# Kernel tuning notes

Hardware: AMD Instinct MI355X
Metric: run time of the kernel (lower is better)

Reference implementation:

```python
import jax, jax.numpy as jnp
import numpy as np
import math

NTOKEN, NINP, NHID, SEQ, BATCH = 33278, 400, 1150, 70, 16
ODE_STEPS = 8  # fixed-step RK4 over t in [0,1] (reference for the adaptive solver)


def lstm_layer(x, h0, c0, Wih, Whh, bih, bhh):
    # x: [S, B, in]; PyTorch gate order i, f, g, o
    def step(carry, xt):
        h, c = carry
        g = xt @ Wih.T + h @ Whh.T + bih + bhh
        i, f, gg, o = jnp.split(g, 4, axis=-1)
        c = jax.nn.sigmoid(f) * c + jax.nn.sigmoid(i) * jnp.tanh(gg)
        h = jax.nn.sigmoid(o) * jnp.tanh(c)
        return (h, c), h
    (hT, cT), ys = jax.lax.scan(step, (h0, c0), x)
    return ys, hT, cT


def cnf_delta_logp(E, cnf_W, cnf_b):
    # ODEnet: f(t,z) = relu(Linear(concat([t, z]))); exact divergence since
    # Jacobian diag = relu'(pre) * diag(Wx). Integrates dz/dt=f, d(dlogp)/dt=-div f.
    wt = cnf_W[:, 0]
    Wx = cnf_W[:, 1:]
    dWx = jnp.diag(Wx)

    def f(t, z):
        pre = z @ Wx.T + t * wt + cnf_b          # [ntoken, ninp]
        div = jnp.sum((pre > 0) * dWx, axis=-1)  # exact trace of df/dz
        return jax.nn.relu(pre), -div

    dt = 1.0 / ODE_STEPS

    def rk4(carry, t):
        z, dl = carry
        k1z, k1l = f(t, z)
        k2z, k2l = f(t + dt / 2, z + dt / 2 * k1z)
        k3z, k3l = f(t + dt / 2, z + dt / 2 * k2z)
        k4z, k4l = f(t + dt, z + dt * k3z)
        z = z + dt / 6 * (k1z + 2 * k2z + 2 * k3z + k4z)
        dl = dl + dt / 6 * (k1l + 2 * k2l + 2 * k3l + k4l)
        return (z, dl), None

    ts = jnp.arange(ODE_STEPS, dtype=E.dtype) * dt
    (zT, dl), _ = jax.lax.scan(rk4, (E, jnp.zeros(E.shape[0], E.dtype)), ts)
    return dl  # [ntoken]


def setup_inputs() -> dict:
    key = jax.random.key(0)
    ks = jax.random.split(key, 16)
    s = 0.1
    inp = {
        "tokens": jax.random.randint(ks[0], (SEQ, BATCH), 0, NTOKEN),
        "h0_0": jnp.zeros((BATCH, NHID), jnp.float32),
        "c0_0": jnp.zeros((BATCH, NHID), jnp.float32),
        "h0_1": jnp.zeros((BATCH, NHID), jnp.float32),
        "c0_1": jnp.zeros((BATCH, NHID), jnp.float32),
        "h0_2": jnp.zeros((BATCH, NINP), jnp.float32),
        "c0_2": jnp.zeros((BATCH, NINP), jnp.float32),
        "emb_W": jax.random.uniform(ks[1], (NTOKEN, NINP), jnp.float32, -s, s),
        "Wih0": jax.random.normal(ks[2], (4 * NHID, NINP), jnp.float32) * 0.02,
        "Whh0": jax.random.normal(ks[3], (4 * NHID, NHID), jnp.float32) * 0.02,
        "bih0": jnp.zeros((4 * NHID,), jnp.float32),
        "bhh0": jnp.zeros((4 * NHID,), jnp.float32),
        "Wih1": jax.random.normal(ks[4], (4 * NHID, NHID), jnp.float32) * 0.02,
        "Whh1": jax.random.normal(ks[5], (4 * NHID, NHID), jnp.float32) * 0.02,
        "bih1": jnp.zeros((4 * NHID,), jnp.float32),
        "bhh1": jnp.zeros((4 * NHID,), jnp.float32),
        "Wih2": jax.random.normal(ks[6], (4 * NINP, NHID), jnp.float32) * 0.02,
        "Whh2": jax.random.normal(ks[7], (4 * NINP, NINP), jnp.float32) * 0.02,
        "bih2": jnp.zeros((4 * NINP,), jnp.float32),
        "bhh2": jnp.zeros((4 * NINP,), jnp.float32),
        "cnf_W": jax.random.normal(ks[8], (NINP, NINP + 1), jnp.float32) * 0.05,
        "cnf_b": jnp.zeros((NINP,), jnp.float32),
    }
    return inp


def reference(tokens, h0_0, c0_0, h0_1, c0_1, h0_2, c0_2, emb_W,
              Wih0, Whh0, bih0, bhh0, Wih1, Whh1, bih1, bhh1,
              Wih2, Whh2, bih2, bhh2, cnf_W, cnf_b):
    # embedding (eval mode: all dropouts are identity)
    x = emb_W[tokens]                               # [S, B, ninp]
    x, h1, c1 = lstm_layer(x, h0_0, c0_0, Wih0, Whh0, bih0, bhh0)
    x, h2, c2 = lstm_layer(x, h0_1, c0_1, Wih1, Whh1, bih1, bhh1)
    x, h3, c3 = lstm_layer(x, h0_2, c0_2, Wih2, Whh2, bih2, bhh2)
    # nhidlast == ninp -> no latent projection
    h = x.reshape(SEQ * BATCH, NINP)

    # MVNLogProb vectorized: -0.5 ||E_v - h_i||^2 - k/2 log(2*pi)
    e2 = jnp.sum(emb_W * emb_W, axis=-1)            # [ntoken]
    h2n = jnp.sum(h * h, axis=-1, keepdims=True)    # [SB, 1]
    sq = e2[None, :] - 2.0 * (h @ emb_W.T) + h2n    # [SB, ntoken]
    log_pz0 = -0.5 * sq - (NINP / 2.0) * math.log(2.0 * math.pi)

    # CNF delta_logp is identical for every token position (loop-invariant)
    delta = cnf_delta_logp(emb_W, cnf_W, cnf_b)     # [ntoken]
    log_pz1 = log_pz0 - delta[None, :]

    prob = jax.nn.softmax(log_pz1, axis=-1)
    log_prob = jnp.log(prob + 1e-8)
    model_output = log_prob.reshape(SEQ, BATCH, NTOKEN)
    return model_output, h1, c1, h2, c2, h3, c3
```

## Files before the change

### kernel.cpp

```cpp
#include <hip/hip_runtime.h>
#include <hip/hip_bf16.h>
#include <math.h>

#define SEQL 70
#define NTOK 33278
#define ODE_STEPS 8
#define NBLK 242
#define NGRP 16
#define CZS 418

typedef __attribute__((ext_vector_type(4))) float f32x4;
typedef __attribute__((ext_vector_type(8))) short s16x8;
typedef unsigned short u16;

__device__ __forceinline__ u16 f2b(float f) {
    union { float f; unsigned int u; } a; a.f = f;
    unsigned int u = a.u;
    return (u16)((u + 0x7FFFu + ((u >> 16) & 1u)) >> 16);
}
__device__ __forceinline__ float b2f(u16 s) {
    union { unsigned int u; float f; } a; a.u = ((unsigned int)s) << 16;
    return a.f;
}

__device__ __forceinline__ unsigned czoff(int row, int colb) {
    unsigned s = ((colb < 768 ? (row & 7) : (row & 3)) << 4);
    return (unsigned)(row * 832 + (colb ^ (int)s));
}

__global__ void cvt_pad_k(const float* __restrict__ src, u16* __restrict__ dst,
                          int G, int Nin, int Nop, int Kin, int Kp, int rs, int co) {
    size_t total = (size_t)G * Nop * Kp;
    for (size_t idx = (size_t)blockIdx.x * 256 + threadIdx.x; idx < total;
         idx += (size_t)gridDim.x * 256) {
        int k = (int)(idx % Kp);
        size_t t2 = idx / Kp;
        int j = (int)(t2 % Nop);
        int g = (int)(t2 / Nop);
        float v = 0.f;
        if (j < Nin && k < Kin) v = src[((size_t)g * Nin + j) * rs + co + k];
        dst[idx] = f2b(v);
// ... 55 lines not shown
                          float* __restrict__ C, int Kp, int lda, int ldb, int ldc,
                          int Mreal, int Nreal, const float* __restrict__ uvec) {
    const int tid = threadIdx.x;
    const int wid = tid >> 6, lane = tid & 63;
    const int la = lane & 15, lk = (lane >> 4) * 8;
    const int m0 = blockIdx.y * 64 + wid * 16;
    const int n0 = blockIdx.x * 64;
    const f32x4 Z4 = {0.f, 0.f, 0.f, 0.f};
    f32x4 acc[4] = {Z4, Z4, Z4, Z4};
    const u16* Ar = A + (size_t)(m0 + la) * lda + lk;
    const u16* Br = B + (size_t)(n0 + la) * ldb + lk;
    for (int k = 0; k < Kp; k += 32) {
        s16x8 a = *(const s16x8*)(Ar + k);
#pragma unroll
        for (int nt = 0; nt < 4; ++nt) {
            s16x8 b = *(const s16x8*)(Br + (size_t)nt * 16 * ldb + k);
            acc[nt] = __builtin_amdgcn_mfma_f32_16x16x32_bf16(a, b, acc[nt], 0, 0, 0);
        }
    }
    const int mr = m0 + (lane >> 4) * 4;
#pragma unroll
    for (int nt = 0; nt < 4; ++nt) {
        int cc = n0 + nt * 16 + la;
        if (cc >= Nreal) continue;
        float uv = uvec ? uvec[cc] : 0.f;
#pragma unroll
        for (int r = 0; r < 4; ++r) {
            int rr = mr + r;
            if (rr < Mreal) C[(size_t)rr * ldc + cc] = acc[nt][r] + uv;
        }
    }
}

__device__ __forceinline__ void gridbar(int* base, int nb, int iter) {
    __syncthreads();
    if (threadIdx.x == 0) {
        int grp = blockIdx.x & (NGRP - 1);
        int gsz = nb / NGRP + ((grp < (nb % NGRP)) ? 1 : 0);
        int* gc   = base + grp * 16;
        int* root = base + 256;
        int* gen  = base + 272;
        int old = __hip_atomic_fetch_add(gc, 1, __ATOMIC_ACQ_REL, __HIP_MEMORY_SCOPE_AGENT);
        if ((old % gsz) == gsz - 1) {
            int r = __hip_atomic_fetch_add(root, 1, __ATOMIC_ACQ_REL, __HIP_MEMORY_SCOPE_AGENT);
            if ((r % NGRP) == NGRP - 1)
                __hip_atomic_fetch_add(gen, 1, __ATOMIC_ACQ_REL, __HIP_MEMORY_SCOPE_AGENT);
        }
        while (__hip_atomic_load(gen, __ATOMIC_RELAXED, __HIP_MEMORY_SCOPE_AGENT) <= iter)
            __builtin_amdgcn_s_sleep(8);
        (void)__hip_atomic_load(gen, __ATOMIC_ACQUIRE, __HIP_MEMORY_SCOPE_AGENT);
    }
    __syncthreads();
}

__global__ __launch_bounds__(768, 3) void lstm_k(
    const float* __restrict__ c00, const float* __restrict__ c01,
    const float* __restrict__ c02,
    const u16* __restrict__ Whh0p, const u16* __restrict__ Wih1p,
    const u16* __restrict__ Whh1p, const u16* __restrict__ Wih2p,
    const u16* __restrict__ Whh2p,
    const float* __restrict__ xW0, const float* __restrict__ bias2v,
    const float* __restrict__ bias1v,
    u16* __restrict__ ys0s, u16* __restrict__ ys1s, u16* __restrict__ ys2s,
    float* __restrict__ oh1, float* __restrict__ oc1,
    float* __restrict__ oh2, float* __restrict__ oc2,
    float* __restrict__ oh3, float* __restrict__ oc3,
    int* __restrict__ bar)
{
    __shared__ __align__(16) char smem[162816];
    u16* wlds = (u16*)smem;
    float* gl = (float*)(smem + 147456);
    const int tid = threadIdx.x;
    const int bid = blockIdx.x;
    const int wv = tid >> 6, lane = tid & 63;
    const int la = lane & 15, lg = lane >> 4;

    int role, jb;
    if (bid < 72) { role = 0; jb = bid; }
    else if (bid < 216) { role = 1; jb = bid - 72; }
    else { role = 2; jb = bid - 216; }

    if (role == 0) {
        for (int s = tid; s < 4 * 36 * 64; s += 768) {
            int ln = s & 63, kt = (s >> 6) % 36, nt = s / (36 * 64);
            int row = nt * 1152 + jb * 16 + (ln & 15);
            int col = kt * 32 + (ln >> 4) * 8;
            *(s16x8*)(wlds + (size_t)s * 8) =
                *(const s16x8*)(Whh0p + (size_t)row * 1152 + col);
        }
    } else if (role == 1) {
        for (int s = tid; s < 2 * 72 * 64; s += 768) {
            int ln = s & 63, kt = (s >> 6) % 72, nt = s / (72 * 64);
            int lr = nt * 16 + (ln & 15);
            int row = (lr >> 3) * 1152 + jb * 8 + (lr & 7);
            int col8 = (ln >> 4) * 8;
            const u16* src = (kt < 36)
                ? Wih1p + (size_t)row * 1152 + kt * 32 + col8
                : Whh1p + (size_t)row * 1152 + (kt - 36) * 32 + col8;
            *(s16x8*)(wlds + (size_t)s * 8) = *(const s16x8*)src;
        }
    }
    __syncthreads();

    float c_reg = 0.f;
    for (int sg = 0; sg < 72; ++sg) {
        int t = sg - role;
        if (t >= 0 && t < SEQL) {
            f32x4 acc = {0.f, 0.f, 0.f, 0.f};
            if (role == 0) {
                int nt = wv / 3, kg = wv - nt * 3;
                const u16* ar = ys0s + ((size_t)sg * 16 + la) * 1152 + lg * 8;
                for (int kt = kg * 12; kt < kg * 12 + 12; ++kt) {
                    s16x8 a = *(const s16x8*)(ar + kt * 32);
                    s16x8 b = *(const s16x8*)(wlds + ((size_t)(nt * 36 + kt) * 64 + lane) * 8);
                    acc = __builtin_amdgcn_mfma_f32_16x16x32_bf16(a, b, acc, 0, 0, 0);
                }
                *(f32x4*)(gl + wv * 320 + la * 20 + lg * 4) = acc;
            } else if (role == 1) {
                int nt = wv / 6, kg = wv - nt * 6;
                const u16* ax = ys0s + ((size_t)sg * 16 + la) * 1152 + lg * 8;
                const u16* ah = ys1s + ((size_t)(sg - 1) * 16 + la) * 1152 + lg * 8;
                for (int kt = kg * 12; kt < kg * 12 + 12; ++kt) {
                    s16x8 a = (kt < 36) ? *(const s16x8*)(ax + kt * 32)
                                        : *(const s16x8*)(ah + (kt - 36) * 32);
                    s16x8 b = *(const s16x8*)(wlds + ((size_t)(nt * 72 + kt) * 64 + lane) * 8);
                    acc = __builtin_amdgcn_mfma_f32_16x16x32_bf16(a, b, acc, 0, 0, 0);
                }
                *(f32x4*)(gl + wv * 320 + la * 20 + lg * 4) = acc;
            } else {
                int nt = wv / 3, kg = wv - nt * 3;
                int k0 = (kg * 49) / 3, k1 = ((kg + 1) * 49) / 3;
                const u16* ax = ys1s + ((size_t)(sg - 1) * 16 + la) * 1152 + lg * 8;
                const u16* ah = ys2s + ((size_t)(sg - 2) * 16 + la) * 416 + lg * 8;
                int wr = nt * 416 + jb * 16 + la;
                for (int kt = k0; kt < k1; ++kt) {
                    s16x8 a, b;
                    if (kt < 36) {
                        a = *(const s16x8*)(ax + kt * 32);
                        b = *(const s16x8*)(Wih2p + (size_t)wr * 1152 + kt * 32 + lg * 8);
                    } else {
                        a = *(const s16x8*)(ah + (kt - 36) * 32);
                        b = *(const s16x8*)(Whh2p + (size_t)wr * 416 + (kt - 36) * 32 + lg * 8);
                    }
                    acc = __builtin_amdgcn_mfma_f32_16x16x32_bf16(a, b, acc, 0, 0, 0);
                }
                *(f32x4*)(gl + wv * 320 + la * 20 + lg * 4) = acc;
            }
            __syncthreads();
            if (role == 1) {
                if (tid < 128) {
                    int u = tid & 7, tb = tid >> 3;
                    int ug = jb * 8 + u;
                    float gv[4];
#pragma unroll
                    for (int g = 0; g < 4; ++g) {
                        int lr = g * 8 + u;
                        int nt = lr >> 4, li = lr & 15;
                        float s = 0.f;
#pragma unroll
                        for (int kg = 0; kg < 6; ++kg)
                            s += gl[(nt * 6 + kg) * 320 + li * 20 + tb];
                        gv[g] = s + bias1v[g * 1152 + ug];
                    }
                    float cprev = (t == 0) ? ((ug < 1150) ? c01[tb * 1150 + ug] : 0.f) : c_reg;
                    float si = 1.f / (1.f + expf(-gv[0]));
                    float sf = 1.f / (1.f + expf(-gv[1]));
                    float so = 1.f / (1.f + expf(-gv[3]));
                    float cn = sf * cprev + si * tanhf(gv[2]);
                    float hn = so * tanhf(cn);
                    c_reg = cn;
                    if (ug < 1150) {
                        ys1s[((size_t)sg * 16 + tb) * 1152 + ug] = f2b(hn);
                        if (t == SEQL - 1) { oh2[tb * 1150 + ug] = hn; oc2[tb * 1150 + ug] = cn; }
                    }
                }
            } else if (tid < 256) {
                int u = tid & 15, tb = tid >> 4;
                int ug = jb * 16 + u;
                float gv[4];
#pragma unroll
                for (int g = 0; g < 4; ++g) {
                    float s = 0.f;
#pragma unroll
                    for (int kg = 0; kg < 3; ++kg)
                        s += gl[(g * 3 + kg) * 320 + u * 20 + tb];
                    gv[g] = s + ((role == 0)
                                 ? xW0[((size_t)t * 16 + tb) * 4608 + g * 1152 + ug]
                                 : bias2v[g * 416 + ug]);
                }
                int N = (role == 0) ? 1150 : 400;
                const float* c0i = (role == 0) ? c00 : c02;
                float cprev = (t == 0) ? ((ug < N) ? c0i[tb * N + ug] : 0.f) : c_reg;
                float si = 1.f / (1.f + expf(-gv[0]));
                float sf = 1.f / (1.f + expf(-gv[1]));
                float so = 1.f / (1.f + expf(-gv[3]));
                float cn = sf * cprev + si * tanhf(gv[2]);
                float hn = so * tanhf(cn);
                c_reg = cn;
                if (ug < N) {
                    if (role == 0) {
                        ys0s[((size_t)(sg + 1) * 16 + tb) * 1152 + ug] = f2b(hn);
                        if (t == SEQL - 1) { oh1[tb * 1150 + ug] = hn; oc1[tb * 1150 + ug] = cn; }
                    } else {
                        ys2s[((size_t)(sg - 1) * 16 + tb) * 416 + ug] = f2b(hn);
                        if (t == SEQL - 1) { oh3[tb * 400 + ug] = hn; oc3[tb * 400 + ug] = cn; }
                    }
                }
            }
        }
        gridbar(bar, NBLK, sg);
    }
}

__global__ __launch_bounds__(512, 2) void cnf_k(const float* __restrict__ emb,
                                                const u16* __restrict__ Wxp,
                                                const float* __restrict__ wt,
                                                const float* __restrict__ bv,
                                                const float* __restrict__ dwx,
                                                float* __restrict__ dl) {
    __shared__ float z0s[64 * CZS];
    __shared__ __align__(16) u16 zi[64 * 416];
    const int tid = threadIdx.x;
    const int m0 = blockIdx.x * 64;

    for (int idx = tid; idx < 64 * 416; idx += 512) {
        int r = idx / 416, cc = idx - r * 416;
        int row = m0 + r;
        float v = (cc < 400 && row < NTOK) ? emb[(size_t)row * 400 + cc] : 0.f;
        if (cc < 416) z0s[r * CZS + cc] = v;
        *(u16*)((char*)zi + czoff(r, cc * 2)) = f2b(v);
    }

    const int wv = tid >> 6, lane = tid & 63;
    const int la = lane & 15, lg = lane >> 4;
    const int lk = lg * 8;
    const int Qw = (wv == 0) ? 4 : 3;
    const int ntb = (wv == 0) ? 0 : 4 + (wv - 1) * 3;

    float wtq[4], bq[4], dwq[4];
#pragma unroll
    for (int q = 0; q < 4; ++q) {
        if (q < Qw) {
            int col = (ntb + q) * 16 + la;
            wtq[q] = wt[col]; bq[q] = bv[col]; dwq[q] = dwx[col];
        } else { wtq[q] = 0.f; bq[q] = 0.f; dwq[q] = 0.f; }
    }
    __syncthreads();

    const float dt = 1.f / ODE_STEPS;
    const f32x4 Z4 = {0.f, 0.f, 0.f, 0.f};
    float Aacc[4][4][4];
#pragma unroll
    for (int m = 0; m < 4; ++m)
#pragma unroll
        for (int q = 0; q < 4; ++q)
#pragma unroll
            for (int r = 0; r < 4; ++r) Aacc[m][q][r] = 0.f;
    float divp[4][4];
#pragma unroll
    for (int m = 0; m < 4; ++m)
#pragma unroll
        for (int r = 0; r < 4; ++r) divp[m][r] = 0.f;

#pragma unroll 1
    for (int st = 0; st < ODE_STEPS; ++st) {
        float t0 = st * dt;
#pragma unroll 1
        for (int s = 0; s < 4; ++s) {
            float ts = t0 + ((s == 0) ? 0.f : (s == 3) ? dt : 0.5f * dt);
            float wgt = (s == 1 || s == 2) ? 2.f : 1.f;
            float cs = (s == 2) ? dt : 0.5f * dt;
            f32x4 pre[4][4];
#pragma unroll
            for (int m = 0; m < 4; ++m)
#pragma unroll
                for (int q = 0; q < 4; ++q) pre[m][q] = Z4;
#pragma unroll 1
            for (int kk = 0; kk < 13; ++kk) {
                s16x8 b[4];
#pragma unroll
                for (int q = 0; q < 4; ++q)
                    if (q < Qw)
                        b[q] = *(const s16x8*)(Wxp + (size_t)((ntb + q) * 16 + la) * 416 +
                                               kk * 32 + lk);
#pragma unroll
                for (int m = 0; m < 4; ++m) {
                    int row = m * 16 + la;
                    s16x8 a = *(const s16x8*)((const char*)zi + czoff(row, (kk * 64 + lg * 16)));
#pragma unroll
                    for (int q = 0; q < 4; ++q)
                        if (q < Qw)
                            pre[m][q] = __builtin_amdgcn_mfma_f32_16x16x32_bf16(
                                a, b[q], pre[m][q], 0, 0, 0);
                }
            }
            __syncthreads();
#pragma unroll
            for (int m = 0; m < 4; ++m) {
#pragma unroll
                for (int q = 0; q < 4; ++q) {
                    if (q >= Qw) continue;
                    int col = (ntb + q) * 16 + la;
#pragma unroll
                    for (int r = 0; r < 4; ++r) {
                        int row = m * 16 + lg * 4 + r;
                        float pv = pre[m][q][r] + ts * wtq[q] + bq[q];
                        float kz = fmaxf(pv, 0.f);
                        if (pv > 0.f) divp[m][r] += dwq[q] * wgt;
                        float An = Aacc[m][q][r] + wgt * kz;
                        float ev;
                        if (s < 3) {
                            Aacc[m][q][r] = An;
                            ev = z0s[row * CZS + col] + cs * kz;
                        } else {
                            float zn = z0s[row * CZS + col] + (dt / 6.f) * An;
                            z0s[row * CZS + col] = zn;
                            Aacc[m][q][r] = 0.f;
                            ev = zn;
                        }
                        *(u16*)((char*)zi + czoff(row, col * 2)) = f2b(ev);
                    }
                }
            }
            __syncthreads();
        }
    }

#pragma unroll
    for (int m = 0; m < 4; ++m)
#pragma unroll
        for (int r = 0; r < 4; ++r) {
            float v = divp[m][r];
            v += __shfl_xor(v, 1, 64);
            v += __shfl_xor(v, 2, 64);
            v += __shfl_xor(v, 4, 64);
            v += __shfl_xor(v, 8, 64);
            divp[m][r] = v;
        }
    float* dsc = (float*)zi;
    if (la == 0) {
#pragma unroll
        for (int m = 0; m < 4; ++m)
#pragma unroll
            for (int r = 0; r < 4; ++r)
                dsc[wv * 64 + m * 16 + lg * 4 + r] = divp[m][r];
    }
    __syncthreads();
    for (int row = tid; row < 64; row += 512) {
        float s = 0.f;
#pragma unroll
        for (int w = 0; w < 8; ++w) s += dsc[w * 64 + row];
        if (m0 + row < NTOK) dl[m0 + row] = -(dt / 6.f) * s;
    }
}

__global__ void logsoftmax_k(float* __restrict__ L, int n) {
    const int row = blockIdx.x;
    float* R = L + (size_t)row * n;
    const int tid = threadIdx.x;
    float mx = -INFINITY, s = 0.f;
    for (int c = tid; c < n; c += 256) {
        float v = R[c];
        float nm = fmaxf(mx, v);
        s = s * expf(mx - nm) + expf(v - nm);
        mx = nm;
    }
#pragma unroll
    for (int off = 1; off < 64; off <<= 1) {
        float om = __shfl_xor(mx, off, 64);
        float os = __shfl_xor(s, off, 64);
        float nm = fmaxf(mx, om);
        s = s * expf(mx - nm) + os * expf(om - nm);
        mx = nm;
    }
    __shared__ float smx[4], ssm[4];
    if ((tid & 63) == 0) { smx[tid >> 6] = mx; ssm[tid >> 6] = s; }
    __syncthreads();
    float bm = fmaxf(fmaxf(smx[0], smx[1]), fmaxf(smx[2], smx[3]));
    float bs = ssm[0] * expf(smx[0] - bm) + ssm[1] * expf(smx[1] - bm) +
               ssm[2] * expf(smx[2] - bm) + ssm[3] * expf(smx[3] - bm);
    float lz = logf(bs);
    for (int c = tid; c < n; c += 256) {
        float v = R[c];
        R[c] = logf(expf(v - bm) + 1e-8f * bs) - lz;
// ... 57 lines not shown
    int*   bar   = (int*)alloc(4096);

    size_t OM = (size_t)SEQL * 16 * NTOK;
    float* oh1 = out + OM;
    float* oc1 = oh1 + 16 * 1150;
    float* oh2 = oc1 + 16 * 1150;
    float* oc2 = oh2 + 16 * 1150;
    float* oh3 = oc2 + 16 * 1150;
    float* oc3 = oh3 + 16 * 400;

    hipMemsetAsync(bar, 0, 4096, stream);
    hipMemsetAsync(ys0s, 0, (size_t)1136 * 1152 * 2, stream);
    hipMemsetAsync(ys1s, 0, (size_t)1136 * 1152 * 2, stream);
    hipMemsetAsync(ys2s, 0, (size_t)1184 * 416 * 2, stream);

    cvt_pad_k<<<2048, 256, 0, stream>>>(Wih0, Wih0p, 4, 1150, 1152, 400, 416, 400, 0);
    cvt_pad_k<<<2048, 256, 0, stream>>>(Whh0, Whh0p, 4, 1150, 1152, 1150, 1152, 1150, 0);
    cvt_pad_k<<<2048, 256, 0, stream>>>(Wih1, Wih1p, 4, 1150, 1152, 1150, 1152, 1150, 0);
    cvt_pad_k<<<2048, 256, 0, stream>>>(Whh1, Whh1p, 4, 1150, 1152, 1150, 1152, 1150, 0);
    cvt_pad_k<<<2048, 256, 0, stream>>>(Wih2, Wih2p, 4, 400, 416, 1150, 1152, 1150, 0);
    cvt_pad_k<<<2048, 256, 0, stream>>>(Whh2, Whh2p, 4, 400, 416, 400, 416, 400, 0);
    cvt_pad_k<<<2048, 256, 0, stream>>>(embW, emb_p, 1, 33278, 33280, 400, 416, 400, 0);
    cvt_pad_k<<<2048, 256, 0, stream>>>(cnfW, Wxp, 1, 400, 416, 400, 416, 401, 1);
    bias_k<<<(4 * 1152 + 255) / 256, 256, 0, stream>>>(bih0, bhh0, bias0, 1150, 1152);
    bias_k<<<(4 * 1152 + 255) / 256, 256, 0, stream>>>(bih1, bhh1, bias1, 1150, 1152);
    bias_k<<<(4 * 416 + 255) / 256, 256, 0, stream>>>(bih2, bhh2, bias2, 400, 416);
    wtdwx_k<<<2, 256, 0, stream>>>(cnfW, wtv, dwx);
    rowsumsq_k<<<NTOK, 64, 0, stream>>>(embW, e2, 400);

    h0cvt_k<<<(16 * 1152 + 255) / 256, 256, 0, stream>>>(h00, ys0s, 1150, 1152);
    h0cvt_k<<<(16 * 1152 + 255) / 256, 256, 0, stream>>>(h01, ys1s, 1150, 1152);
    h0cvt_k<<<(16 * 416 + 255) / 256, 256, 0, stream>>>(h02, ys2s, 400, 416);

    cnf_k<<<520, 512, 0, stream>>>(embW, Wxp, wtv, cnfb, dwx, dl);
    ucomb_k<<<(NTOK + 255) / 256, 256, 0, stream>>>(e2, dl, uvec);

    embed_k<<<(1152 * 416 + 255) / 256, 256, 0, stream>>>(tokens, embW, x0);
    gemm_bt_k<<<dim3(72, 18), 256, 0, stream>>>(x0, Wih0p, xW, 416, 416, 416, 4608,
                                                1120, 4608, bias0);

    lstm_k<<<NBLK, 768, 0, stream>>>(
        c00, c01, c02, Whh0p, Wih1p, Whh1p, Wih2p, Whh2p,
        xW, bias2, bias1, ys0s, ys1s, ys2s,
        oh1, oc1, oh2, oc2, oh3, oc3, bar);

    gemm_bt_k<<<dim3(520, 18), 256, 0, stream>>>(ys2s + (size_t)16 * 416, emb_p, out,
                                                 416, 416, 416, NTOK, 1120, NTOK, uvec);
    logsoftmax_k<<<1120, 256, 0, stream>>>(out, NTOK);
}
```

Baseline: 2.998 ms.

## Replace global grid barrier with per-role barriers and generation-based dataflow waits

The LSTM persistent kernel drops the single grid-wide barrier per wavefront step. Each layer role now gets its own hierarchical barrier, and downstream layers spin on the upstream role's generation counter. Layers can therefore run ahead of one another instead of marching in lockstep. Separately, the CNF kernel uses 32-row tiles with twice as many blocks and a higher occupancy bound, to improve parallelism. The risks are ordering bugs: there is no back-pressure from downstream layers and the barrier-counter layout is new.

New measurement: 3.188 ms. 6.3% more time.

```diff
diff --git a/kernel.cpp b/kernel.cpp
--- a/kernel.cpp
+++ b/kernel.cpp
@@ -6,7 +6,6 @@
 #define NTOK 33278
 #define ODE_STEPS 8
 #define NBLK 242
-#define NGRP 16
 #define CZS 418
 
 typedef __attribute__((ext_vector_type(4))) float f32x4;
@@ -128,22 +127,30 @@
     }
 }
 
-__device__ __forceinline__ void gridbar(int* base, int nb, int iter) {
+__device__ __forceinline__ void rolebar(int* base, int nb, int ngrp, int roleBlk, int iter) {
     __syncthreads();
     if (threadIdx.x == 0) {
-        int grp = blockIdx.x & (NGRP - 1);
-        int gsz = nb / NGRP + ((grp < (nb % NGRP)) ? 1 : 0);
+        int grp = roleBlk % ngrp;
+        int gsz = nb / ngrp + ((grp < (nb % ngrp)) ? 1 : 0);
         int* gc   = base + grp * 16;
-        int* root = base + 256;
-        int* gen  = base + 272;
+        int* root = base + ngrp * 16;
+        int* gen  = base + ngrp * 16 + 16;
         int old = __hip_atomic_fetch_add(gc, 1, __ATOMIC_ACQ_REL, __HIP_MEMORY_SCOPE_AGENT);
         if ((old % gsz) == gsz - 1) {
             int r = __hip_atomic_fetch_add(root, 1, __ATOMIC_ACQ_REL, __HIP_MEMORY_SCOPE_AGENT);
-            if ((r % NGRP) == NGRP - 1)
+            if ((r % ngrp) == ngrp - 1)
                 __hip_atomic_fetch_add(gen, 1, __ATOMIC_ACQ_REL, __HIP_MEMORY_SCOPE_AGENT);
         }
         while (__hip_atomic_load(gen, __ATOMIC_RELAXED, __HIP_MEMORY_SCOPE_AGENT) <= iter)
-            __builtin_amdgcn_s_sleep(8);
+            __builtin_amdgcn_s_sleep(4);
+        (void)__hip_atomic_load(gen, __ATOMIC_ACQUIRE, __HIP_MEMORY_SCOPE_AGENT);
+    }
+    __syncthreads();
+}
+__device__ __forceinline__ void waitgen(int* gen, int needed) {
+    if (threadIdx.x == 0) {
+        while (__hip_atomic_load(gen, __ATOMIC_RELAXED, __HIP_MEMORY_SCOPE_AGENT) < needed)
+            __builtin_amdgcn_s_sleep(4);
         (void)__hip_atomic_load(gen, __ATOMIC_ACQUIRE, __HIP_MEMORY_SCOPE_AGENT);
     }
     __syncthreads();
@@ -176,6 +183,12 @@
     else if (bid < 216) { role = 1; jb = bid - 72; }
     else { role = 2; jb = bid - 216; }
 
+    int* bar0 = bar;
+    int* bar1 = bar + 256;
+    int* bar2 = bar + 768;
+    int* g0 = bar0 + 144;
+    int* g1 = bar1 + 272;
+
     if (role == 0) {
         for (int s = tid; s < 4 * 36 * 64; s += 768) {
             int ln = s & 63, kt = (s >> 6) % 36, nt = s / (36 * 64);
@@ -199,127 +212,129 @@
     __syncthreads();
 
     float c_reg = 0.f;
-    for (int sg = 0; sg < 72; ++sg) {
-        int t = sg - role;
-        if (t >= 0 && t < SEQL) {
-            f32x4 acc = {0.f, 0.f, 0.f, 0.f};
-            if (role == 0) {
-                int nt = wv / 3, kg = wv - nt * 3;
-                const u16* ar = ys0s + ((size_t)sg * 16 + la) * 1152 + lg * 8;
-                for (int kt = kg * 12; kt < kg * 12 + 12; ++kt) {
-                    s16x8 a = *(const s16x8*)(ar + kt * 32);
-                    s16x8 b = *(const s16x8*)(wlds + ((size_t)(nt * 36 + kt) * 64 + lane) * 8);
-                    acc = __builtin_amdgcn_mfma_f32_16x16x32_bf16(a, b, acc, 0, 0, 0);
+    for (int t = 0; t < SEQL; ++t) {
+        if (role == 1) waitgen(g0, t + 1);
+        else if (role == 2) waitgen(g1, t + 1);
+
+        f32x4 acc = {0.f, 0.f, 0.f, 0.f};
+        if (role == 0) {
+            int nt = wv / 3, kg = wv - nt * 3;
+            const u16* ar = ys0s + ((size_t)t * 16 + la) * 1152 + lg * 8;
+            for (int kt = kg * 12; kt < kg * 12 + 12; ++kt) {
+                s16x8 a = *(const s16x8*)(ar + kt * 32);
+                s16x8 b = *(const s16x8*)(wlds + ((size_t)(nt * 36 + kt) * 64 + lane) * 8);
+                acc = __builtin_amdgcn_mfma_f32_16x16x32_bf16(a, b, acc, 0, 0, 0);
+            }
+            *(f32x4*)(gl + wv * 320 + la * 20 + lg * 4) = acc;
+        } else if (role == 1) {
+            int nt = wv / 6, kg = wv - nt * 6;
+            const u16* ax = ys0s + ((size_t)(t + 1) * 16 + la) * 1152 + lg * 8;
+            const u16* ah = ys1s + ((size_t)t * 16 + la) * 1152 + lg * 8;
+            for (int kt = kg * 12; kt < kg * 12 + 12; ++kt) {
+                s16x8 a = (kt < 36) ? *(const s16x8*)(ax + kt * 32)
+                                    : *(const s16x8*)(ah + (kt - 36) * 32);
+                s16x8 b = *(const s16x8*)(wlds + ((size_t)(nt * 72 + kt) * 64 + lane) * 8);
+                acc = __builtin_amdgcn_mfma_f32_16x16x32_bf16(a, b, acc, 0, 0, 0);
+            }
+            *(f32x4*)(gl + wv * 320 + la * 20 + lg * 4) = acc;
+        } else {
+            int nt = wv / 3, kg = wv - nt * 3;
+            int k0 = (kg * 49) / 3, k1 = ((kg + 1) * 49) / 3;
+            const u16* ax = ys1s + ((size_t)(t + 1) * 16 + la) * 1152 + lg * 8;
+            const u16* ah = ys2s + ((size_t)t * 16 + la) * 416 + lg * 8;
+            int wr = nt * 416 + jb * 16 + la;
+            for (int kt = k0; kt < k1; ++kt) {
+                s16x8 a, b;
+                if (kt < 36) {
+                    a = *(const s16x8*)(ax + kt * 32);
+                    b = *(const s16x8*)(Wih2p + (size_t)wr * 1152 + kt * 32 + lg * 8);
+                } else {
+                    a = *(const s16x8*)(ah + (kt - 36) * 32);
+                    b = *(const s16x8*)(Whh2p + (size_t)wr * 416 + (kt - 36) * 32 + lg * 8);
                 }
-                *(f32x4*)(gl + wv * 320 + la * 20 + lg * 4) = acc;
-            } else if (role == 1) {
-                int nt = wv / 6, kg = wv - nt * 6;
-                const u16* ax = ys0s + ((size_t)sg * 16 + la) * 1152 + lg * 8;
-                const u16* ah = ys1s + ((size_t)(sg - 1) * 16 + la) * 1152 + lg * 8;
-                for (int kt = kg * 12; kt < kg * 12 + 12; ++kt) {
-                    s16x8 a = (kt < 36) ? *(const s16x8*)(ax + kt * 32)
-                                        : *(const s16x8*)(ah + (kt - 36) * 32);
-                    s16x8 b = *(const s16x8*)(wlds + ((size_t)(nt * 72 + kt) * 64 + lane) * 8);
-                    acc = __builtin_amdgcn_mfma_f32_16x16x32_bf16(a, b, acc, 0, 0, 0);
+                acc = __builtin_amdgcn_mfma_f32_16x16x32_bf16(a, b, acc, 0, 0, 0);
+            }
+            *(f32x4*)(gl + wv * 320 + la * 20 + lg * 4) = acc;
+        }
+        __syncthreads();
+        if (role == 1) {
+            if (tid < 128) {
+                int u = tid & 7, tb = tid >> 3;
+                int ug = jb * 8 + u;
+                float gv[4];
+#pragma unroll
+                for (int g = 0; g < 4; ++g) {
+                    int lr = g * 8 + u;
+                    int nt = lr >> 4, li = lr & 15;
+                    float s = 0.f;
+#pragma unroll
+                    for (int kg = 0; kg < 6; ++kg)
+                        s += gl[(nt * 6 + kg) * 320 + li * 20 + tb];
+                    gv[g] = s + bias1v[g * 1152 + ug];
                 }
-                *(f32x4*)(gl + wv * 320 + la * 20 + lg * 4) = acc;
-            } else {
-                int nt = wv / 3, kg = wv - nt * 3;
-                int k0 = (kg * 49) / 3, k1 = ((kg + 1) * 49) / 3;
-                const u16* ax = ys1s + ((size_t)(sg - 1) * 16 + la) * 1152 + lg * 8;
-                const u16* ah = ys2s + ((size_t)(sg - 2) * 16 + la) * 416 + lg * 8;
-                int wr = nt * 416 + jb * 16 + la;
-                for (int kt = k0; kt < k1; ++kt) {
-                    s16x8 a, b;
-                    if (kt < 36) {
-                        a = *(const s16x8*)(ax + kt * 32);
-                        b = *(const s16x8*)(Wih2p + (size_t)wr * 1152 + kt * 32 + lg * 8);
-                    } else {
-                        a = *(const s16x8*)(ah + (kt - 36) * 32);
-                        b = *(const s16x8*)(Whh2p + (size_t)wr * 416 + (kt - 36) * 32 + lg * 8);
-                    }
-                    acc = __builtin_amdgcn_mfma_f32_16x16x32_bf16(a, b, acc, 0, 0, 0);
-                }
-                *(f32x4*)(gl + wv * 320 + la * 20 + lg * 4) = acc;
-            }
-            __syncthreads();
-            if (role == 1) {
-                if (tid < 128) {
-                    int u = tid & 7, tb = tid >> 3;
-                    int ug = jb * 8 + u;
-                    float gv[4];
-#pragma unroll
-                    for (int g = 0; g < 4; ++g) {
-                        int lr = g * 8 + u;
-                        int nt = lr >> 4, li = lr & 15;
-                        float s = 0.f;
-#pragma unroll
-                        for (int kg = 0; kg < 6; ++kg)
-                            s += gl[(nt * 6 + kg) * 320 + li * 20 + tb];
-                        gv[g] = s + bias1v[g * 1152 + ug];
-                    }
-                    float cprev = (t == 0) ? ((ug < 1150) ? c01[tb * 1150 + ug] : 0.f) : c_reg;
-                    float si = 1.f / (1.f + expf(-gv[0]));
-                    float sf = 1.f / (1.f + expf(-gv[1]));
-                    float so = 1.f / (1.f + expf(-gv[3]));
-                    float cn = sf * cprev + si * tanhf(gv[2]);
-                    float hn = so * tanhf(cn);
-                    c_reg = cn;
-                    if (ug < 1150) {
-                        ys1s[((size_t)sg * 16 + tb) * 1152 + ug] = f2b(hn);
-                        if (t == SEQL - 1) { oh2[tb * 1150 + ug] = hn; oc2[tb * 1150 + ug] = cn; }
-                    }
-                }
-            } else if (tid < 256) {
-                int u = tid & 15, tb = tid >> 4;
-                int ug = jb * 16 + u;
-                float gv[4];
-#pragma unroll
-                for (int g = 0; g < 4; ++g) {
-                    float s = 0.f;
-#pragma unroll
-                    for (int kg = 0; kg < 3; ++kg)
-                        s += gl[(g * 3 + kg) * 320 + u * 20 + tb];
-                    gv[g] = s + ((role == 0)
-                                 ? xW0[((size_t)t * 16 + tb) * 4608 + g * 1152 + ug]
-                                 : bias2v[g * 416 + ug]);
-                }
-                int N = (role == 0) ? 1150 : 400;
-                const float* c0i = (role == 0) ? c00 : c02;
-                float cprev = (t == 0) ? ((ug < N) ? c0i[tb * N + ug] : 0.f) : c_reg;
+                float cprev = (t == 0) ? ((ug < 1150) ? c01[tb * 1150 + ug] : 0.f) : c_reg;
                 float si = 1.f / (1.f + expf(-gv[0]));
                 float sf = 1.f / (1.f + expf(-gv[1]));
                 float so = 1.f / (1.f + expf(-gv[3]));
                 float cn = sf * cprev + si * tanhf(gv[2]);
                 float hn = so * tanhf(cn);
                 c_reg = cn;
-                if (ug < N) {
-                    if (role == 0) {
-                        ys0s[((size_t)(sg + 1) * 16 + tb) * 1152 + ug] = f2b(hn);
-                        if (t == SEQL - 1) { oh1[tb * 1150 + ug] = hn; oc1[tb * 1150 + ug] = cn; }
-                    } else {
-                        ys2s[((size_t)(sg - 1) * 16 + tb) * 416 + ug] = f2b(hn);
-                        if (t == SEQL - 1) { oh3[tb * 400 + ug] = hn; oc3[tb * 400 + ug] = cn; }
-                    }
+                if (ug < 1150) {
+                    ys1s[((size_t)(t + 1) * 16 + tb) * 1152 + ug] = f2b(hn);
+                    if (t == SEQL - 1) { oh2[tb * 1150 + ug] = hn; oc2[tb * 1150 + ug] = cn; }
                 }
             }
-        }
-        gridbar(bar, NBLK, sg);
-    }
-}
-
-__global__ __launch_bounds__(512, 2) void cnf_k(const float* __restrict__ emb,
+        } else if (tid < 256) {
+            int u = tid & 15, tb = tid >> 4;
+            int ug = jb * 16 + u;
+            float gv[4];
+#pragma unroll
+            for (int g = 0; g < 4; ++g) {
+                float s = 0.f;
+#pragma unroll
+                for (int kg = 0; kg < 3; ++kg)
+                    s += gl[(g * 3 + kg) * 320 + u * 20 + tb];
+                gv[g] = s + ((role == 0)
+                             ? xW0[((size_t)t * 16 + tb) * 4608 + g * 1152 + ug]
+                             : bias2v[g * 416 + ug]);
+            }
+            int N = (role == 0) ? 1150 : 400;
+            const float* c0i = (role == 0) ? c00 : c02;
+            float cprev = (t == 0) ? ((ug < N) ? c0i[tb * N + ug] : 0.f) : c_reg;
+            float si = 1.f / (1.f + expf(-gv[0]));
+            float sf = 1.f / (1.f + expf(-gv[1]));
+            float so = 1.f / (1.f + expf(-gv[3]));
+            float cn = sf * cprev + si * tanhf(gv[2]);
+            float hn = so * tanhf(cn);
+            c_reg = cn;
+            if (ug < N) {
+                if (role == 0) {
+                    ys0s[((size_t)(t + 1) * 16 + tb) * 1152 + ug] = f2b(hn);
+                    if (t == SEQL - 1) { oh1[tb * 1150 + ug] = hn; oc1[tb * 1150 + ug] = cn; }
+                } else {
+                    ys2s[((size_t)(t + 1) * 16 + tb) * 416 + ug] = f2b(hn);
+                    if (t == SEQL - 1) { oh3[tb * 400 + ug] = hn; oc3[tb * 400 + ug] = cn; }
+                }
+            }
+        }
+        if (role == 0) rolebar(bar0, 72, 8, jb, t);
+        else if (role == 1) rolebar(bar1, 144, 16, jb, t);
+        else rolebar(bar2, 26, 1, jb, t);
+    }
+}
+
+__global__ __launch_bounds__(512, 4) void cnf_k(const float* __restrict__ emb,
                                                 const u16* __restrict__ Wxp,
                                                 const float* __restrict__ wt,
                                                 const float* __restrict__ bv,
                                                 const float* __restrict__ dwx,
                                                 float* __restrict__ dl) {
-    __shared__ float z0s[64 * CZS];
-    __shared__ __align__(16) u16 zi[64 * 416];
+    __shared__ float z0s[32 * CZS];
+    __shared__ __align__(16) u16 zi[32 * 416];
     const int tid = threadIdx.x;
-    const int m0 = blockIdx.x * 64;
-
-    for (int idx = tid; idx < 64 * 416; idx += 512) {
+    const int m0 = blockIdx.x * 32;
+
+    for (int idx = tid; idx < 32 * 416; idx += 512) {
         int r = idx / 416, cc = idx - r * 416;
         int row = m0 + r;
         float v = (cc < 400 && row < NTOK) ? emb[(size_t)row * 400 + cc] : 0.f;
@@ -345,16 +360,16 @@
 
     const float dt = 1.f / ODE_STEPS;
     const f32x4 Z4 = {0.f, 0.f, 0.f, 0.f};
-    float Aacc[4][4][4];
-#pragma unroll
-    for (int m = 0; m < 4; ++m)
+    float Aacc[2][4][4];
+#pragma unroll
+    for (int m = 0; m < 2; ++m)
 #pragma unroll
         for (int q = 0; q < 4; ++q)
 #pragma unroll
             for (int r = 0; r < 4; ++r) Aacc[m][q][r] = 0.f;
-    float divp[4][4];
-#pragma unroll
-    for (int m = 0; m < 4; ++m)
+    float divp[2][4];
+#pragma unroll
+    for (int m = 0; m < 2; ++m)
 #pragma unroll
         for (int r = 0; r < 4; ++r) divp[m][r] = 0.f;
 
@@ -366,9 +381,9 @@
             float ts = t0 + ((s == 0) ? 0.f : (s == 3) ? dt : 0.5f * dt);
             float wgt = (s == 1 || s == 2) ? 2.f : 1.f;
             float cs = (s == 2) ? dt : 0.5f * dt;
-            f32x4 pre[4][4];
-#pragma unroll
-            for (int m = 0; m < 4; ++m)
+            f32x4 pre[2][4];
+#pragma unroll
+            for (int m = 0; m < 2; ++m)
 #pragma unroll
                 for (int q = 0; q < 4; ++q) pre[m][q] = Z4;
 #pragma unroll 1
@@ -380,9 +395,9 @@
                         b[q] = *(const s16x8*)(Wxp + (size_t)((ntb + q) * 16 + la) * 416 +
                                                kk * 32 + lk);
 #pragma unroll
-                for (int m = 0; m < 4; ++m) {
+                for (int m = 0; m < 2; ++m) {
                     int row = m * 16 + la;
-                    s16x8 a = *(const s16x8*)((const char*)zi + czoff(row, (kk * 64 + lg * 16)));
+                    s16x8 a = *(const s16x8*)((const char*)zi + czoff(row, kk * 64 + lg * 16));
 #pragma unroll
                     for (int q = 0; q < 4; ++q)
                         if (q < Qw)
@@ -392,7 +407,7 @@
             }
             __syncthreads();
 #pragma unroll
-            for (int m = 0; m < 4; ++m) {
+            for (int m = 0; m < 2; ++m) {
 #pragma unroll
                 for (int q = 0; q < 4; ++q) {
                     if (q >= Qw) continue;
@@ -423,7 +438,7 @@
     }
 
 #pragma unroll
-    for (int m = 0; m < 4; ++m)
+    for (int m = 0; m < 2; ++m)
 #pragma unroll
         for (int r = 0; r < 4; ++r) {
             float v = divp[m][r];
@@ -436,16 +451,16 @@
     float* dsc = (float*)zi;
     if (la == 0) {
 #pragma unroll
-        for (int m = 0; m < 4; ++m)
+        for (int m = 0; m < 2; ++m)
 #pragma unroll
             for (int r = 0; r < 4; ++r)
-                dsc[wv * 64 + m * 16 + lg * 4 + r] = divp[m][r];
+                dsc[wv * 32 + m * 16 + lg * 4 + r] = divp[m][r];
     }
     __syncthreads();
-    for (int row = tid; row < 64; row += 512) {
+    for (int row = tid; row < 32; row += 512) {
         float s = 0.f;
 #pragma unroll
-        for (int w = 0; w < 8; ++w) s += dsc[w * 64 + row];
+        for (int w = 0; w < 8; ++w) s += dsc[w * 32 + row];
         if (m0 + row < NTOK) dl[m0 + row] = -(dt / 6.f) * s;
     }
 }
@@ -569,7 +584,7 @@
     h0cvt_k<<<(16 * 1152 + 255) / 256, 256, 0, stream>>>(h01, ys1s, 1150, 1152);
     h0cvt_k<<<(16 * 416 + 255) / 256, 256, 0, stream>>>(h02, ys2s, 400, 416);
 
-    cnf_k<<<520, 512, 0, stream>>>(embW, Wxp, wtv, cnfb, dwx, dl);
+    cnf_k<<<1040, 512, 0, stream>>>(embW, Wxp, wtv, cnfb, dwx, dl);
     ucomb_k<<<(NTOK + 255) / 256, 256, 0, stream>>>(e2, dl, uvec);
 
     embed_k<<<(1152 * 416 + 255) / 256, 256, 0, stream>>>(tokens, embW, x0);
```

## Replace global grid barrier with per-layer barriers and flag waits; widen CNF blocks

Applied to the files above, without the earlier changes.

The LSTM wavefront kernel drops its single hierarchical grid barrier across all 242 blocks. Each layer role now has its own flat barrier, and downstream layers spin on the upstream layer's generation counter, so layers can run ahead in a pipelined way instead of stepping in lockstep. The sleep interval is also shortened. Separately, the CNF kernel moves from 512 to 1024 threads per block, with fewer column tiles per wave. The barrier change relies on correct memory ordering across per-role counters, and the barrier buffer must be laid out and zeroed for the new counter offsets.

Measured after the change: 2.993 ms. No clear change (-0.2%).

```diff
diff --git a/kernel.cpp b/kernel.cpp
--- a/kernel.cpp
+++ b/kernel.cpp
@@ -6,7 +6,6 @@
 #define NTOK 33278
 #define ODE_STEPS 8
 #define NBLK 242
-#define NGRP 16
 #define CZS 418
 
 typedef __attribute__((ext_vector_type(4))) float f32x4;
@@ -128,22 +127,22 @@
     }
 }
 
-__device__ __forceinline__ void gridbar(int* base, int nb, int iter) {
+__device__ __forceinline__ void flatbar(int* cnt, int* gen, int nb, int iter) {
     __syncthreads();
     if (threadIdx.x == 0) {
-        int grp = blockIdx.x & (NGRP - 1);
-        int gsz = nb / NGRP + ((grp < (nb % NGRP)) ? 1 : 0);
-        int* gc   = base + grp * 16;
-        int* root = base + 256;
-        int* gen  = base + 272;
-        int old = __hip_atomic_fetch_add(gc, 1, __ATOMIC_ACQ_REL, __HIP_MEMORY_SCOPE_AGENT);
-        if ((old % gsz) == gsz - 1) {
-            int r = __hip_atomic_fetch_add(root, 1, __ATOMIC_ACQ_REL, __HIP_MEMORY_SCOPE_AGENT);
-            if ((r % NGRP) == NGRP - 1)
-                __hip_atomic_fetch_add(gen, 1, __ATOMIC_ACQ_REL, __HIP_MEMORY_SCOPE_AGENT);
-        }
+        int old = __hip_atomic_fetch_add(cnt, 1, __ATOMIC_ACQ_REL, __HIP_MEMORY_SCOPE_AGENT);
+        if ((old % nb) == nb - 1)
+            __hip_atomic_fetch_add(gen, 1, __ATOMIC_ACQ_REL, __HIP_MEMORY_SCOPE_AGENT);
         while (__hip_atomic_load(gen, __ATOMIC_RELAXED, __HIP_MEMORY_SCOPE_AGENT) <= iter)
-            __builtin_amdgcn_s_sleep(8);
+            __builtin_amdgcn_s_sleep(2);
+        (void)__hip_atomic_load(gen, __ATOMIC_ACQUIRE, __HIP_MEMORY_SCOPE_AGENT);
+    }
+    __syncthreads();
+}
+__device__ __forceinline__ void waitgen(int* gen, int needed) {
+    if (threadIdx.x == 0) {
+        while (__hip_atomic_load(gen, __ATOMIC_RELAXED, __HIP_MEMORY_SCOPE_AGENT) < needed)
+            __builtin_amdgcn_s_sleep(2);
         (void)__hip_atomic_load(gen, __ATOMIC_ACQUIRE, __HIP_MEMORY_SCOPE_AGENT);
     }
     __syncthreads();
@@ -176,6 +175,10 @@
     else if (bid < 216) { role = 1; jb = bid - 72; }
     else { role = 2; jb = bid - 216; }
 
+    int* c0 = bar;        int* g0 = bar + 16;
+    int* c1 = bar + 32;   int* g1 = bar + 48;
+    int* c2 = bar + 64;   int* g2 = bar + 80;
+
     if (role == 0) {
         for (int s = tid; s < 4 * 36 * 64; s += 768) {
             int ln = s & 63, kt = (s >> 6) % 36, nt = s / (36 * 64);
@@ -199,145 +202,147 @@
     __syncthreads();
 
     float c_reg = 0.f;
-    for (int sg = 0; sg < 72; ++sg) {
-        int t = sg - role;
-        if (t >= 0 && t < SEQL) {
-            f32x4 acc = {0.f, 0.f, 0.f, 0.f};
-            if (role == 0) {
-                int nt = wv / 3, kg = wv - nt * 3;
-                const u16* ar = ys0s + ((size_t)sg * 16 + la) * 1152 + lg * 8;
-                for (int kt = kg * 12; kt < kg * 12 + 12; ++kt) {
-                    s16x8 a = *(const s16x8*)(ar + kt * 32);
-                    s16x8 b = *(const s16x8*)(wlds + ((size_t)(nt * 36 + kt) * 64 + lane) * 8);
-                    acc = __builtin_amdgcn_mfma_f32_16x16x32_bf16(a, b, acc, 0, 0, 0);
+    for (int t = 0; t < SEQL; ++t) {
+        if (role == 1) waitgen(g0, t + 1);
+        else if (role == 2) waitgen(g1, t + 1);
+
+        f32x4 acc = {0.f, 0.f, 0.f, 0.f};
+        if (role == 0) {
+            int nt = wv / 3, kg = wv - nt * 3;
+            const u16* ar = ys0s + ((size_t)t * 16 + la) * 1152 + lg * 8;
+            for (int kt = kg * 12; kt < kg * 12 + 12; ++kt) {
+                s16x8 a = *(const s16x8*)(ar + kt * 32);
+                s16x8 b = *(const s16x8*)(wlds + ((size_t)(nt * 36 + kt) * 64 + lane) * 8);
+                acc = __builtin_amdgcn_mfma_f32_16x16x32_bf16(a, b, acc, 0, 0, 0);
+            }
+            *(f32x4*)(gl + wv * 320 + la * 20 + lg * 4) = acc;
+        } else if (role == 1) {
+            int nt = wv / 6, kg = wv - nt * 6;
+            const u16* ax = ys0s + ((size_t)(t + 1) * 16 + la) * 1152 + lg * 8;
+            const u16* ah = ys1s + ((size_t)t * 16 + la) * 1152 + lg * 8;
+            for (int kt = kg * 12; kt < kg * 12 + 12; ++kt) {
+                s16x8 a = (kt < 36) ? *(const s16x8*)(ax + kt * 32)
+                                    : *(const s16x8*)(ah + (kt - 36) * 32);
+                s16x8 b = *(const s16x8*)(wlds + ((size_t)(nt * 72 + kt) * 64 + lane) * 8);
+                acc = __builtin_amdgcn_mfma_f32_16x16x32_bf16(a, b, acc, 0, 0, 0);
+            }
+            *(f32x4*)(gl + wv * 320 + la * 20 + lg * 4) = acc;
+        } else {
+            int nt = wv / 3, kg = wv - nt * 3;
+            int k0 = (kg * 49) / 3, k1 = ((kg + 1) * 49) / 3;
+            const u16* ax = ys1s + ((size_t)(t + 1) * 16 + la) * 1152 + lg * 8;
+            const u16* ah = ys2s + ((size_t)t * 16 + la) * 416 + lg * 8;
+            int wr = nt * 416 + jb * 16 + la;
+            for (int kt = k0; kt < k1; ++kt) {
+                s16x8 a, b;
+                if (kt < 36) {
+                    a = *(const s16x8*)(ax + kt * 32);
+                    b = *(const s16x8*)(Wih2p + (size_t)wr * 1152 + kt * 32 + lg * 8);
+                } else {
+                    a = *(const s16x8*)(ah + (kt - 36) * 32);
+                    b = *(const s16x8*)(Whh2p + (size_t)wr * 416 + (kt - 36) * 32 + lg * 8);
                 }
-                *(f32x4*)(gl + wv * 320 + la * 20 + lg * 4) = acc;
-            } else if (role == 1) {
-                int nt = wv / 6, kg = wv - nt * 6;
-                const u16* ax = ys0s + ((size_t)sg * 16 + la) * 1152 + lg * 8;
-                const u16* ah = ys1s + ((size_t)(sg - 1) * 16 + la) * 1152 + lg * 8;
-                for (int kt = kg * 12; kt < kg * 12 + 12; ++kt) {
-                    s16x8 a = (kt < 36) ? *(const s16x8*)(ax + kt * 32)
-                                        : *(const s16x8*)(ah + (kt - 36) * 32);
-                    s16x8 b = *(const s16x8*)(wlds + ((size_t)(nt * 72 + kt) * 64 + lane) * 8);
-                    acc = __builtin_amdgcn_mfma_f32_16x16x32_bf16(a, b, acc, 0, 0, 0);
+                acc = __builtin_amdgcn_mfma_f32_16x16x32_bf16(a, b, acc, 0, 0, 0);
+            }
+            *(f32x4*)(gl + wv * 320 + la * 20 + lg * 4) = acc;
+        }
+        __syncthreads();
+        if (role == 1) {
+            if (tid < 128) {
+                int u = tid & 7, tb = tid >> 3;
+                int ug = jb * 8 + u;
+                float gv[4];
+#pragma unroll
+                for (int g = 0; g < 4; ++g) {
+                    int lr = g * 8 + u;
+                    int nt = lr >> 4, li = lr & 15;
+                    float s = 0.f;
+#pragma unroll
+                    for (int kg = 0; kg < 6; ++kg)
+                        s += gl[(nt * 6 + kg) * 320 + li * 20 + tb];
+                    gv[g] = s + bias1v[g * 1152 + ug];
                 }
-                *(f32x4*)(gl + wv * 320 + la * 20 + lg * 4) = acc;
-            } else {
-                int nt = wv / 3, kg = wv - nt * 3;
-                int k0 = (kg * 49) / 3, k1 = ((kg + 1) * 49) / 3;
-                const u16* ax = ys1s + ((size_t)(sg - 1) * 16 + la) * 1152 + lg * 8;
-                const u16* ah = ys2s + ((size_t)(sg - 2) * 16 + la) * 416 + lg * 8;
-                int wr = nt * 416 + jb * 16 + la;
-                for (int kt = k0; kt < k1; ++kt) {
-                    s16x8 a, b;
-                    if (kt < 36) {
-                        a = *(const s16x8*)(ax + kt * 32);
-                        b = *(const s16x8*)(Wih2p + (size_t)wr * 1152 + kt * 32 + lg * 8);
-                    } else {
-                        a = *(const s16x8*)(ah + (kt - 36) * 32);
-                        b = *(const s16x8*)(Whh2p + (size_t)wr * 416 + (kt - 36) * 32 + lg * 8);
-                    }
-                    acc = __builtin_amdgcn_mfma_f32_16x16x32_bf16(a, b, acc, 0, 0, 0);
-                }
-                *(f32x4*)(gl + wv * 320 + la * 20 + lg * 4) = acc;
-            }
-            __syncthreads();
-            if (role == 1) {
-                if (tid < 128) {
-                    int u = tid & 7, tb = tid >> 3;
-                    int ug = jb * 8 + u;
-                    float gv[4];
-#pragma unroll
-                    for (int g = 0; g < 4; ++g) {
-                        int lr = g * 8 + u;
-                        int nt = lr >> 4, li = lr & 15;
-                        float s = 0.f;
-#pragma unroll
-                        for (int kg = 0; kg < 6; ++kg)
-                            s += gl[(nt * 6 + kg) * 320 + li * 20 + tb];
-                        gv[g] = s + bias1v[g * 1152 + ug];
-                    }
-                    float cprev = (t == 0) ? ((ug < 1150) ? c01[tb * 1150 + ug] : 0.f) : c_reg;
-                    float si = 1.f / (1.f + expf(-gv[0]));
-                    float sf = 1.f / (1.f + expf(-gv[1]));
-                    float so = 1.f / (1.f + expf(-gv[3]));
-                    float cn = sf * cprev + si * tanhf(gv[2]);
-                    float hn = so * tanhf(cn);
-                    c_reg = cn;
-                    if (ug < 1150) {
-                        ys1s[((size_t)sg * 16 + tb) * 1152 + ug] = f2b(hn);
-                        if (t == SEQL - 1) { oh2[tb * 1150 + ug] = hn; oc2[tb * 1150 + ug] = cn; }
-                    }
-                }
-            } else if (tid < 256) {
-                int u = tid & 15, tb = tid >> 4;
-                int ug = jb * 16 + u;
-                float gv[4];
-#pragma unroll
-                for (int g = 0; g < 4; ++g) {
-                    float s = 0.f;
-#pragma unroll
-                    for (int kg = 0; kg < 3; ++kg)
-                        s += gl[(g * 3 + kg) * 320 + u * 20 + tb];
-                    gv[g] = s + ((role == 0)
-                                 ? xW0[((size_t)t * 16 + tb) * 4608 + g * 1152 + ug]
-                                 : bias2v[g * 416 + ug]);
-                }
-                int N = (role == 0) ? 1150 : 400;
-                const float* c0i = (role == 0) ? c00 : c02;
-                float cprev = (t == 0) ? ((ug < N) ? c0i[tb * N + ug] : 0.f) : c_reg;
+                float cprev = (t == 0) ? ((ug < 1150) ? c01[tb * 1150 + ug] : 0.f) : c_reg;
                 float si = 1.f / (1.f + expf(-gv[0]));
                 float sf = 1.f / (1.f + expf(-gv[1]));
                 float so = 1.f / (1.f + expf(-gv[3]));
                 float cn = sf * cprev + si * tanhf(gv[2]);
                 float hn = so * tanhf(cn);
                 c_reg = cn;
-                if (ug < N) {
-                    if (role == 0) {
-                        ys0s[((size_t)(sg + 1) * 16 + tb) * 1152 + ug] = f2b(hn);
-                        if (t == SEQL - 1) { oh1[tb * 1150 + ug] = hn; oc1[tb * 1150 + ug] = cn; }
-                    } else {
-                        ys2s[((size_t)(sg - 1) * 16 + tb) * 416 + ug] = f2b(hn);
-                        if (t == SEQL - 1) { oh3[tb * 400 + ug] = hn; oc3[tb * 400 + ug] = cn; }
-                    }
+                if (ug < 1150) {
+                    ys1s[((size_t)(t + 1) * 16 + tb) * 1152 + ug] = f2b(hn);
+                    if (t == SEQL - 1) { oh2[tb * 1150 + ug] = hn; oc2[tb * 1150 + ug] = cn; }
                 }
             }
-        }
-        gridbar(bar, NBLK, sg);
-    }
-}
-
-__global__ __launch_bounds__(512, 2) void cnf_k(const float* __restrict__ emb,
-                                                const u16* __restrict__ Wxp,
-                                                const float* __restrict__ wt,
-                                                const float* __restrict__ bv,
-                                                const float* __restrict__ dwx,
-                                                float* __restrict__ dl) {
+        } else if (tid < 256) {
+            int u = tid & 15, tb = tid >> 4;
+            int ug = jb * 16 + u;
+            float gv[4];
+#pragma unroll
+            for (int g = 0; g < 4; ++g) {
+                float s = 0.f;
+#pragma unroll
+                for (int kg = 0; kg < 3; ++kg)
+                    s += gl[(g * 3 + kg) * 320 + u * 20 + tb];
+                gv[g] = s + ((role == 0)
+                             ? xW0[((size_t)t * 16 + tb) * 4608 + g * 1152 + ug]
+                             : bias2v[g * 416 + ug]);
+            }
+            int N = (role == 0) ? 1150 : 400;
+            const float* c0i = (role == 0) ? c00 : c02;
+            float cprev = (t == 0) ? ((ug < N) ? c0i[tb * N + ug] : 0.f) : c_reg;
+            float si = 1.f / (1.f + expf(-gv[0]));
+            float sf = 1.f / (1.f + expf(-gv[1]));
+            float so = 1.f / (1.f + expf(-gv[3]));
+            float cn = sf * cprev + si * tanhf(gv[2]);
+            float hn = so * tanhf(cn);
+            c_reg = cn;
+            if (ug < N) {
+                if (role == 0) {
+                    ys0s[((size_t)(t + 1) * 16 + tb) * 1152 + ug] = f2b(hn);
+                    if (t == SEQL - 1) { oh1[tb * 1150 + ug] = hn; oc1[tb * 1150 + ug] = cn; }
+                } else {
+                    ys2s[((size_t)(t + 1) * 16 + tb) * 416 + ug] = f2b(hn);
+                    if (t == SEQL - 1) { oh3[tb * 400 + ug] = hn; oc3[tb * 400 + ug] = cn; }
+                }
+            }
+        }
+        if (role == 0) flatbar(c0, g0, 72, t);
+        else if (role == 1) flatbar(c1, g1, 144, t);
+        else flatbar(c2, g2, 26, t);
+    }
+}
+
+__global__ __launch_bounds__(1024, 4) void cnf_k(const float* __restrict__ emb,
+                                                 const u16* __restrict__ Wxp,
+                                                 const float* __restrict__ wt,
+                                                 const float* __restrict__ bv,
+                                                 const float* __restrict__ dwx,
+                                                 float* __restrict__ dl) {
     __shared__ float z0s[64 * CZS];
     __shared__ __align__(16) u16 zi[64 * 416];
     const int tid = threadIdx.x;
     const int m0 = blockIdx.x * 64;
 
-    for (int idx = tid; idx < 64 * 416; idx += 512) {
+    for (int idx = tid; idx < 64 * 416; idx += 1024) {
         int r = idx / 416, cc = idx - r * 416;
         int row = m0 + r;
         float v = (cc < 400 && row < NTOK) ? emb[(size_t)row * 400 + cc] : 0.f;
-        if (cc < 416) z0s[r * CZS + cc] = v;
+        z0s[r * CZS + cc] = v;
         *(u16*)((char*)zi + czoff(r, cc * 2)) = f2b(v);
     }
 
     const int wv = tid >> 6, lane = tid & 63;
     const int la = lane & 15, lg = lane >> 4;
     const int lk = lg * 8;
-    const int Qw = (wv == 0) ? 4 : 3;
-    const int ntb = (wv == 0) ? 0 : 4 + (wv - 1) * 3;
-
-    float wtq[4], bq[4], dwq[4];
-#pragma unroll
-    for (int q = 0; q < 4; ++q) {
+    const int tb0 = (wv * 25) >> 4;
+    const int Qw = (((wv + 1) * 25) >> 4) - tb0;
+
+    float wtq[2], bq[2], dwq[2];
+#pragma unroll
+    for (int q = 0; q < 2; ++q) {
         if (q < Qw) {
-            int col = (ntb + q) * 16 + la;
+            int col = (tb0 + q) * 16 + la;
             wtq[q] = wt[col]; bq[q] = bv[col]; dwq[q] = dwx[col];
         } else { wtq[q] = 0.f; bq[q] = 0.f; dwq[q] = 0.f; }
     }
@@ -345,11 +350,11 @@
 
     const float dt = 1.f / ODE_STEPS;
     const f32x4 Z4 = {0.f, 0.f, 0.f, 0.f};
-    float Aacc[4][4][4];
+    float Aacc[4][2][4];
 #pragma unroll
     for (int m = 0; m < 4; ++m)
 #pragma unroll
-        for (int q = 0; q < 4; ++q)
+        for (int q = 0; q < 2; ++q)
 #pragma unroll
             for (int r = 0; r < 4; ++r) Aacc[m][q][r] = 0.f;
     float divp[4][4];
@@ -366,25 +371,25 @@
             float ts = t0 + ((s == 0) ? 0.f : (s == 3) ? dt : 0.5f * dt);
             float wgt = (s == 1 || s == 2) ? 2.f : 1.f;
             float cs = (s == 2) ? dt : 0.5f * dt;
-            f32x4 pre[4][4];
+            f32x4 pre[4][2];
 #pragma unroll
             for (int m = 0; m < 4; ++m)
 #pragma unroll
-                for (int q = 0; q < 4; ++q) pre[m][q] = Z4;
+                for (int q = 0; q < 2; ++q) pre[m][q] = Z4;
 #pragma unroll 1
             for (int kk = 0; kk < 13; ++kk) {
-                s16x8 b[4];
-#pragma unroll
-                for (int q = 0; q < 4; ++q)
+                s16x8 b[2];
+#pragma unroll
+                for (int q = 0; q < 2; ++q)
                     if (q < Qw)
-                        b[q] = *(const s16x8*)(Wxp + (size_t)((ntb + q) * 16 + la) * 416 +
+                        b[q] = *(const s16x8*)(Wxp + (size_t)((tb0 + q) * 16 + la) * 416 +
                                                kk * 32 + lk);
 #pragma unroll
                 for (int m = 0; m < 4; ++m) {
                     int row = m * 16 + la;
-                    s16x8 a = *(const s16x8*)((const char*)zi + czoff(row, (kk * 64 + lg * 16)));
-#pragma unroll
-                    for (int q = 0; q < 4; ++q)
+                    s16x8 a = *(const s16x8*)((const char*)zi + czoff(row, kk * 64 + lg * 16));
+#pragma unroll
+                    for (int q = 0; q < 2; ++q)
                         if (q < Qw)
                             pre[m][q] = __builtin_amdgcn_mfma_f32_16x16x32_bf16(
                                 a, b[q], pre[m][q], 0, 0, 0);
@@ -394,9 +399,9 @@
 #pragma unroll
             for (int m = 0; m < 4; ++m) {
 #pragma unroll
-                for (int q = 0; q < 4; ++q) {
+                for (int q = 0; q < 2; ++q) {
                     if (q >= Qw) continue;
-                    int col = (ntb + q) * 16 + la;
+                    int col = (tb0 + q) * 16 + la;
 #pragma unroll
                     for (int r = 0; r < 4; ++r) {
                         int row = m * 16 + lg * 4 + r;
@@ -442,10 +447,10 @@
                 dsc[wv * 64 + m * 16 + lg * 4 + r] = divp[m][r];
     }
     __syncthreads();
-    for (int row = tid; row < 64; row += 512) {
+    for (int row = tid; row < 64; row += 1024) {
         float s = 0.f;
 #pragma unroll
-        for (int w = 0; w < 8; ++w) s += dsc[w * 64 + row];
+        for (int w = 0; w < 16; ++w) s += dsc[w * 64 + row];
         if (m0 + row < NTOK) dl[m0 + row] = -(dt / 6.f) * s;
     }
 }
@@ -569,7 +574,7 @@
     h0cvt_k<<<(16 * 1152 + 255) / 256, 256, 0, stream>>>(h01, ys1s, 1150, 1152);
     h0cvt_k<<<(16 * 416 + 255) / 256, 256, 0, stream>>>(h02, ys2s, 400, 416);
 
-    cnf_k<<<520, 512, 0, stream>>>(embW, Wxp, wtv, cnfb, dwx, dl);
+    cnf_k<<<520, 1024, 0, stream>>>(embW, Wxp, wtv, cnfb, dwx, dl);
     ucomb_k<<<(NTOK + 255) / 256, 256, 0, stream>>>(e2, dl, uvec);
 
     embed_k<<<(1152 * 416 + 255) / 256, 256, 0, stream>>>(tokens, embW, x0);
```
